# Kernel optimization log

Hardware: AMD Instinct MI355X
Metric: run time of the kernel (lower is better)

## Reference

```python
import jax, jax.numpy as jnp
import numpy as np

B, S, H, NH = 8, 2048, 128, 4
HS = H // NH
EPS = 1e-8


def setup_inputs() -> dict:
    key = jax.random.key(0)
    ks = jax.random.split(key, 20)
    sc = 1.0 / np.sqrt(H)
    d = {
        'item_embeds': jax.random.normal(ks[0], (B, S, H), jnp.float32),
        'behavior_embeds': jax.random.normal(ks[1], (B, S, H), jnp.float32),
        'attn_mask': jnp.zeros((B, 1, S, S), jnp.float32),
    }
    names = ['Wq', 'Wk', 'Wv', 'Wqb', 'Wkb', 'Wvb', 'Wf']
    for i, n in enumerate(names):
        d[n] = jax.random.normal(ks[2 + i], (H, H), jnp.float32) * sc
        d['b' + n[1:]] = jnp.zeros((H,), jnp.float32)
    d['ln_w'] = jnp.ones((H,), jnp.float32)
    d['ln_b'] = jnp.zeros((H,), jnp.float32)
    return d


def _split_heads(x):
    # [B,S,H] -> [B,NH,S,HS]
    return x.reshape(B, S, NH, HS).transpose(0, 2, 1, 3)


def _layer_norm(x, w, b):
    u = jnp.mean(x, -1, keepdims=True)
    s = jnp.mean((x - u) ** 2, -1, keepdims=True)
    return w * ((x - u) / jnp.sqrt(s + EPS)) + b


def reference(item_embeds, behavior_embeds, attn_mask,
              Wq, bq, Wk, bk, Wv, bv,
              Wqb, bqb, Wkb, bkb, Wvb, bvb,
              Wf, bf, ln_w, ln_b):
    Q = _split_heads(item_embeds @ Wq + bq)
    K = _split_heads(item_embeds @ Wk + bk)
    V = _split_heads(item_embeds @ Wv + bv)
    Qb = _split_heads(behavior_embeds @ Wqb + bqb)
    Kb = _split_heads(behavior_embeds @ Wkb + bkb)
    # V_behavior computed in the original forward but unused downstream
    _Vb = _split_heads(behavior_embeds @ Wvb + bvb)
    scores = (jnp.einsum('bhqd,bhkd->bhqk', Q, K)
              + jnp.einsum('bhqd,bhkd->bhqk', Qb, Kb)) / np.sqrt(HS)
    scores = scores + attn_mask
    probs = jax.nn.softmax(scores, axis=-1)
    attn_out = jnp.einsum('bhqk,bhkd->bhqd', probs, V)
    attn_out = attn_out.transpose(0, 2, 1, 3).reshape(B, S, H)
    out = attn_out @ Wf + bf
    return _layer_norm(out + item_embeds, ln_w, ln_b)
```

## Files before the change

kernel.cpp:

```cpp
#include <hip/hip_runtime.h>
#include <math.h>

typedef unsigned short ushort_t;
typedef __attribute__((ext_vector_type(8))) short bf16x8;
typedef __attribute__((ext_vector_type(4))) float f32x4;

namespace {
constexpr int B = 8, S = 2048, H = 128, NH = 4, HS = 32;
constexpr float EPS = 1e-8f;
constexpr float SCALE = 0.17677669529663687f;
constexpr int QT = 32, KT = 64;
constexpr int NE = B * S * H;
}

__device__ __forceinline__ ushort_t f2bf(float f) {
  unsigned u = __float_as_uint(f);
  unsigned r = (u + 0x7FFFu + ((u >> 16) & 1u)) >> 16;
  return (ushort_t)r;
}

__device__ __forceinline__ f32x4 mfma16(bf16x8 a, bf16x8 b, f32x4 c) {
  return __builtin_amdgcn_mfma_f32_16x16x32_bf16(a, b, c, 0, 0, 0);
}

__global__ __launch_bounds__(256) void wcvt_kernel(
    const float* __restrict__ Wq, const float* __restrict__ Wk, const float* __restrict__ Wv,
    const float* __restrict__ Wqb, const float* __restrict__ Wkb, const float* __restrict__ Wf,
    ushort_t* __restrict__ Wt)
{
  const float* Ws[6] = {Wq, Wk, Wv, Wqb, Wkb, Wf};
  const int m = blockIdx.y;
  const int kb = blockIdx.x;
  const float* W = Ws[m];
  __shared__ float T[32 * 132];
  const int t = threadIdx.x;
#pragma unroll
  for (int u = 0; u < 4; ++u) {
    const int idx = u * 256 + t;
    const int row = idx >> 5, c4 = idx & 31;
    const float4 v = *(const float4*)&W[(kb * 32 + row) * H + c4 * 4];
    *(float4*)&T[row * 132 + c4 * 4] = v;
  }
  __syncthreads();
#pragma unroll
  for (int u = 0; u < 16; ++u) {
    const int idx = u * 256 + t;
    const int n = idx >> 5, kk = idx & 31;
    Wt[m * (H * H) + n * H + kb * 32 + kk] = f2bf(T[kk * 132 + n]);
  }
}

__global__ __launch_bounds__(256) void proj_kernel(
    const float* __restrict__ item, const float* __restrict__ beh,
    const ushort_t* __restrict__ Wt,
    const float* __restrict__ bq, const float* __restrict__ bk, const float* __restrict__ bv,
    const float* __restrict__ bqb, const float* __restrict__ bkb,
    ushort_t* __restrict__ Qo, ushort_t* __restrict__ Ko, ushort_t* __restrict__ Qbo,
    ushort_t* __restrict__ Kbo, ushort_t* __restrict__ Vto)
{
  __shared__ ushort_t Xi[64 * 136];
  __shared__ ushort_t Xb[64 * 136];
  const int t = threadIdx.x;
  const long r0 = (long)blockIdx.x * 64;
#pragma unroll
  for (int u = 0; u < 8; ++u) {
    const int idx = u * 256 + t;
    const int row = idx >> 5, c4 = idx & 31;
    const float4 vi = *(const float4*)&item[(r0 + row) * H + c4 * 4];
    const float4 vb = *(const float4*)&beh[(r0 + row) * H + c4 * 4];
    unsigned long long pi = (unsigned long long)f2bf(vi.x) | ((unsigned long long)f2bf(vi.y) << 16)
        | ((unsigned long long)f2bf(vi.z) << 32) | ((unsigned long long)f2bf(vi.w) << 48);
    unsigned long long pb = (unsigned long long)f2bf(vb.x) | ((unsigned long long)f2bf(vb.y) << 16)
        | ((unsigned long long)f2bf(vb.z) << 32) | ((unsigned long long)f2bf(vb.w) << 48);
    *(unsigned long long*)&Xi[row * 136 + c4 * 4] = pi;
    *(unsigned long long*)&Xb[row * 136 + c4 * 4] = pb;
  }
  __syncthreads();

  const int w = t >> 6, l = t & 63, l15 = l & 15, quad = l >> 4;
  const int bb = (int)(r0 >> 11);
  const int s0 = (int)(r0 & (S - 1));
  const float* bias[5] = {bq, bk, bv, bqb, bkb};
  ushort_t* dsts[5] = {Qo, Ko, Vto, Qbo, Kbo};

  bf16x8 af[4][4];
#pragma unroll
  for (int mt = 0; mt < 4; ++mt)
#pragma unroll
    for (int ks = 0; ks < 4; ++ks)
      af[mt][ks] = *(const bf16x8*)&Xi[(mt * 16 + l15) * 136 + ks * 32 + quad * 8];

  for (int p = 0; p < 5; ++p) {
    if (p == 3) {
#pragma unroll
      for (int mt = 0; mt < 4; ++mt)
#pragma unroll
        for (int ks = 0; ks < 4; ++ks)
          af[mt][ks] = *(const bf16x8*)&Xb[(mt * 16 + l15) * 136 + ks * 32 + quad * 8];
    }
    f32x4 acc[4][2];
    float bcol[2];
#pragma unroll
    for (int nt = 0; nt < 2; ++nt) {
      bcol[nt] = bias[p][w * 32 + nt * 16 + l15];
#pragma unroll
      for (int mt = 0; mt < 4; ++mt)
        acc[mt][nt] = (f32x4){bcol[nt], bcol[nt], bcol[nt], bcol[nt]};
    }
    const ushort_t* Wp = Wt + p * (H * H);
#pragma unroll
    for (int ks = 0; ks < 4; ++ks) {
      bf16x8 bfr[2];
#pragma unroll
      for (int nt = 0; nt < 2; ++nt)
        bfr[nt] = *(const bf16x8*)&Wp[(w * 32 + nt * 16 + l15) * H + ks * 32 + quad * 8];
#pragma unroll
      for (int mt = 0; mt < 4; ++mt)
#pragma unroll
        for (int nt = 0; nt < 2; ++nt)
          acc[mt][nt] = mfma16(af[mt][ks], bfr[nt], acc[mt][nt]);
    }
    ushort_t* dst = dsts[p];
#pragma unroll
    for (int mt = 0; mt < 4; ++mt)
#pragma unroll
      for (int nt = 0; nt < 2; ++nt)
#pragma unroll
        for (int r = 0; r < 4; ++r) {
          const int s = s0 + mt * 16 + quad * 4 + r;
          const int d = nt * 16 + l15;
          long idx;
          if (p == 2)
            idx = ((long)(bb * NH + w) * HS + d) * S + s;
          else
            idx = ((long)(bb * NH + w) * S + s) * HS + d;
          dst[idx] = f2bf(acc[mt][nt][r]);
        }
  }
}

__global__ __launch_bounds__(256) void attn_kernel(
    const ushort_t* __restrict__ Q, const ushort_t* __restrict__ K,
    const ushort_t* __restrict__ Qb, const ushort_t* __restrict__ Kb,
    const ushort_t* __restrict__ Vt, const float* __restrict__ mask,
    ushort_t* __restrict__ attn_out)
{
  __shared__ ushort_t Pb[NH][32 * 72];
  const int t = threadIdx.x;
  const int w = t >> 6;
  const int l = t & 63, l15 = l & 15, quad = l >> 4;
  const int q0 = blockIdx.x * QT;
  const int b = blockIdx.y;
  const long hQ = (long)(b * NH + w) * S * HS;
  const long hV = (long)(b * NH + w) * HS * S;

  bf16x8 qf[2], qbf[2];
#pragma unroll
  for (int mt = 0; mt < 2; ++mt) {
    qf[mt]  = *(const bf16x8*)&Q[hQ + (long)(q0 + mt * 16 + l15) * HS + quad * 8];
    qbf[mt] = *(const bf16x8*)&Qb[hQ + (long)(q0 + mt * 16 + l15) * HS + quad * 8];
  }
  const float* mbase[2][4];
#pragma unroll
  for (int mt = 0; mt < 2; ++mt)
#pragma unroll
    for (int r = 0; r < 4; ++r)
      mbase[mt][r] = mask + ((long)b * S + q0 + mt * 16 + quad * 4 + r) * S + l15;

  float mold[2][4], lsum[2][4];
  f32x4 O[2][2];
#pragma unroll
  for (int mt = 0; mt < 2; ++mt) {
#pragma unroll
    for (int r = 0; r < 4; ++r) { mold[mt][r] = -1e30f; lsum[mt][r] = 0.f; }
#pragma unroll
    for (int dt = 0; dt < 2; ++dt) O[mt][dt] = (f32x4){0.f, 0.f, 0.f, 0.f};
  }
  ushort_t* Pw = Pb[w];

  for (int kt = 0; kt < S / KT; ++kt) {
    const int k0 = kt * KT;
    float mk[2][4][4];
#pragma unroll
    for (int mt = 0; mt < 2; ++mt)
#pragma unroll
      for (int r = 0; r < 4; ++r)
#pragma unroll
        for (int nt = 0; nt < 4; ++nt)
          mk[mt][nt][r] = mbase[mt][r][k0 + nt * 16];
    bf16x8 kf[4], kbf[4], vf[2][2];
#pragma unroll
    for (int nt = 0; nt < 4; ++nt) {
      kf[nt]  = *(const bf16x8*)&K[hQ + (long)(k0 + nt * 16 + l15) * HS + quad * 8];
      kbf[nt] = *(const bf16x8*)&Kb[hQ + (long)(k0 + nt * 16 + l15) * HS + quad * 8];
    }
#pragma unroll
    for (int dt = 0; dt < 2; ++dt)
#pragma unroll
      for (int ks = 0; ks < 2; ++ks)
        vf[dt][ks] = *(const bf16x8*)&Vt[hV + (long)(dt * 16 + l15) * S + k0 + ks * 32 + quad * 8];

    f32x4 sc[2][4];
#pragma unroll
    for (int mt = 0; mt < 2; ++mt)
#pragma unroll
      for (int nt = 0; nt < 4; ++nt) {
        f32x4 z = (f32x4){0.f, 0.f, 0.f, 0.f};
        z = mfma16(qf[mt], kf[nt], z);
        z = mfma16(qbf[mt], kbf[nt], z);
        sc[mt][nt] = z;
      }
#pragma unroll
    for (int mt = 0; mt < 2; ++mt)
#pragma unroll
      for (int nt = 0; nt < 4; ++nt)
#pragma unroll
        for (int r = 0; r < 4; ++r)
          sc[mt][nt][r] = sc[mt][nt][r] * SCALE + mk[mt][nt][r];
    float alpha[2][4];
#pragma unroll
    for (int mt = 0; mt < 2; ++mt)
#pragma unroll
      for (int r = 0; r < 4; ++r) {
        float rm = fmaxf(fmaxf(sc[mt][0][r], sc[mt][1][r]), fmaxf(sc[mt][2][r], sc[mt][3][r]));
        rm = fmaxf(rm, __shfl_xor(rm, 1));
        rm = fmaxf(rm, __shfl_xor(rm, 2));
        rm = fmaxf(rm, __shfl_xor(rm, 4));
        rm = fmaxf(rm, __shfl_xor(rm, 8));
        const float mnew = fmaxf(mold[mt][r], rm);
        alpha[mt][r] = __expf(mold[mt][r] - mnew);
        float rs = 0.f;
#pragma unroll
        for (int nt = 0; nt < 4; ++nt) {
          const float p = __expf(sc[mt][nt][r] - mnew);
          sc[mt][nt][r] = p;
          rs += p;
        }
        rs += __shfl_xor(rs, 1);
        rs += __shfl_xor(rs, 2);
        rs += __shfl_xor(rs, 4);
        rs += __shfl_xor(rs, 8);
        lsum[mt][r] = lsum[mt][r] * alpha[mt][r] + rs;
        mold[mt][r] = mnew;
      }
#pragma unroll
    for (int mt = 0; mt < 2; ++mt)
#pragma unroll
      for (int dt = 0; dt < 2; ++dt)
#pragma unroll
        for (int r = 0; r < 4; ++r)
          O[mt][dt][r] *= alpha[mt][r];
#pragma unroll
    for (int mt = 0; mt < 2; ++mt)
#pragma unroll
      for (int nt = 0; nt < 4; ++nt)
#pragma unroll
        for (int r = 0; r < 4; ++r)
          Pw[(mt * 16 + quad * 4 + r) * 72 + nt * 16 + l15] = f2bf(sc[mt][nt][r]);
#pragma unroll
    for (int mt = 0; mt < 2; ++mt) {
      bf16x8 pf[2];
#pragma unroll
      for (int ks = 0; ks < 2; ++ks)
        pf[ks] = *(const bf16x8*)&Pw[(mt * 16 + l15) * 72 + ks * 32 + quad * 8];
#pragma unroll
      for (int dt = 0; dt < 2; ++dt)
#pragma unroll
        for (int ks = 0; ks < 2; ++ks)
          O[mt][dt] = mfma16(pf[ks], vf[dt][ks], O[mt][dt]);
    }
  }
#pragma unroll
  for (int mt = 0; mt < 2; ++mt)
#pragma unroll
    for (int r = 0; r < 4; ++r) {
      const float inv = 1.f / lsum[mt][r];
      const long row = (long)b * S + q0 + mt * 16 + quad * 4 + r;
#pragma unroll
      for (int dt = 0; dt < 2; ++dt)
        attn_out[row * H + w * 32 + dt * 16 + l15] = f2bf(O[mt][dt][r] * inv);
    }
}

__global__ __launch_bounds__(256) void out_kernel(
    const ushort_t* __restrict__ attn, const float* __restrict__ item,
    const ushort_t* __restrict__ Wft, const float* __restrict__ bf_,
    const float* __restrict__ lnw, const float* __restrict__ lnb,
    float* __restrict__ out)
{
  __shared__ ushort_t As[64 * 136];
  __shared__ float Ys[64 * 132];
  const int t = threadIdx.x;
  const long r0 = (long)blockIdx.x * 64;
#pragma unroll
  for (int u = 0; u < 4; ++u) {
    const int idx = u * 256 + t;
    const int row = idx >> 4, c8 = idx & 15;
    *(uint4*)&As[row * 136 + c8 * 8] = *(const uint4*)&attn[(r0 + row) * H + c8 * 8];
  }
  __syncthreads();
  const int w = t >> 6, l = t & 63, l15 = l & 15, quad = l >> 4;
  f32x4 acc[4][2];
#pragma unroll
  for (int nt = 0; nt < 2; ++nt) {
    const float bcol = bf_[w * 32 + nt * 16 + l15];
#pragma unroll
    for (int mt = 0; mt < 4; ++mt)
      acc[mt][nt] = (f32x4){bcol, bcol, bcol, bcol};
  }
#pragma unroll
  for (int ks = 0; ks < 4; ++ks) {
    bf16x8 bfr[2];
#pragma unroll
    for (int nt = 0; nt < 2; ++nt)
      bfr[nt] = *(const bf16x8*)&Wft[(w * 32 + nt * 16 + l15) * H + ks * 32 + quad * 8];
#pragma unroll
    for (int mt = 0; mt < 4; ++mt) {
      const bf16x8 a = *(const bf16x8*)&As[(mt * 16 + l15) * 136 + ks * 32 + quad * 8];
      for (int nt = 0; nt < 2; ++nt)
        acc[mt][nt] = mfma16(a, bfr[nt], acc[mt][nt]);
    }
  }
#pragma unroll
  for (int mt = 0; mt < 4; ++mt)
#pragma unroll
    for (int nt = 0; nt < 2; ++nt)
#pragma unroll
      for (int r = 0; r < 4; ++r) {
        const int rl = mt * 16 + quad * 4 + r;
        const int col = w * 32 + nt * 16 + l15;
        Ys[rl * 132 + col] = acc[mt][nt][r] + item[(r0 + rl) * H + col];
      }
  __syncthreads();
  const int rl = t >> 2, ch = t & 3;
  float v[32];
#pragma unroll
  for (int g = 0; g < 8; ++g) {
    const float4 y = *(const float4*)&Ys[rl * 132 + ch * 32 + g * 4];
    v[g * 4 + 0] = y.x; v[g * 4 + 1] = y.y; v[g * 4 + 2] = y.z; v[g * 4 + 3] = y.w;
  }
  float s = 0.f;
#pragma unroll
  for (int i = 0; i < 32; ++i) s += v[i];
  s += __shfl_xor(s, 1);
  s += __shfl_xor(s, 2);
  const float u_ = s * (1.f / H);
  float s2 = 0.f;
#pragma unroll
  for (int i = 0; i < 32; ++i) { const float d = v[i] - u_; s2 += d * d; }
  s2 += __shfl_xor(s2, 1);
  s2 += __shfl_xor(s2, 2);
  const float rinv = rsqrtf(s2 * (1.f / H) + EPS);
#pragma unroll
  for (int g = 0; g < 8; ++g) {
    float4 o;
    const int col = ch * 32 + g * 4;
    o.x = lnw[col + 0] * ((v[g * 4 + 0] - u_) * rinv) + lnb[col + 0];
    o.y = lnw[col + 1] * ((v[g * 4 + 1] - u_) * rinv) + lnb[col + 1];
    o.z = lnw[col + 2] * ((v[g * 4 + 2] - u_) * rinv) + lnb[col + 2];
    o.w = lnw[col + 3] * ((v[g * 4 + 3] - u_) * rinv) + lnb[col + 3];
    *(float4*)&out[(r0 + rl) * H + col] = o;
  }
}

extern "C" void kernel_launch(void* const* d_in, const int* in_sizes, int n_in,
                              void* d_out, int out_size, void* d_ws, size_t ws_size,
                              hipStream_t stream) {
  const float* item = (const float*)d_in[0];
  const float* beh  = (const float*)d_in[1];
  const float* mask = (const float*)d_in[2];
  const float* Wq  = (const float*)d_in[3];  const float* bq  = (const float*)d_in[4];
  const float* Wk  = (const float*)d_in[5];  const float* bk  = (const float*)d_in[6];
  const float* Wv  = (const float*)d_in[7];  const float* bv  = (const float*)d_in[8];
  const float* Wqb = (const float*)d_in[9];  const float* bqb = (const float*)d_in[10];
  const float* Wkb = (const float*)d_in[11]; const float* bkb = (const float*)d_in[12];
  const float* Wf  = (const float*)d_in[15]; const float* bfv = (const float*)d_in[16];
  const float* lnw = (const float*)d_in[17]; const float* lnb = (const float*)d_in[18];
  float* out = (float*)d_out;

  ushort_t* ws = (ushort_t*)d_ws;
  ushort_t* Qw   = ws;
  ushort_t* Kw   = Qw + NE;
  ushort_t* Qbw  = Kw + NE;
  ushort_t* Kbw  = Qbw + NE;
  ushort_t* Vtw  = Kbw + NE;
  ushort_t* Attw = Vtw + NE;
  ushort_t* Wt   = Attw + NE;

  wcvt_kernel<<<dim3(4, 6), 256, 0, stream>>>(Wq, Wk, Wv, Wqb, Wkb, Wf, Wt);
  proj_kernel<<<dim3((B * S) / 64), 256, 0, stream>>>(
      item, beh, Wt, bq, bk, bv, bqb, bkb, Qw, Kw, Qbw, Kbw, Vtw);
  attn_kernel<<<dim3(S / QT, B), 256, 0, stream>>>(
      Qw, Kw, Qbw, Kbw, Vtw, mask, Attw);
  out_kernel<<<dim3((B * S) / 64), 256, 0, stream>>>(
      Attw, item, Wt + 5 * H * H, bfv, lnw, lnb, out);
}
```

Before: 380.9 us.

## Halve tile rows, fold softmax scale into weights, stage projection stores via LDS

The attention query tile drops from 32 to 16 rows, with launch bounds requesting 4 blocks per CU, so more blocks run and each uses fewer registers. The 1/sqrt(HS) scale is folded into the Wq/Wqb weights and their biases, and the mask is preloaded into the MFMA accumulator, which removes the per-score multiply-add. The projection kernel now handles 32 rows per block, keeps both input fragments resident, and stages results in LDS so global stores are 16-byte coalesced, including the transposed V. The output kernel also moves to 32-row tiles. In exchange, K/V and mask reads are repeated across twice as many query blocks, and the projection adds extra barriers.

Measured after the change: 379.4 us. Within noise of the previous version (-0.4%).

```diff
diff --git a/kernel.cpp b/kernel.cpp
--- a/kernel.cpp
+++ b/kernel.cpp
@@ -9,7 +9,7 @@
 constexpr int B = 8, S = 2048, H = 128, NH = 4, HS = 32;
 constexpr float EPS = 1e-8f;
 constexpr float SCALE = 0.17677669529663687f;
-constexpr int QT = 32, KT = 64;
+constexpr int QT = 16, KT = 64;
 constexpr int NE = B * S * H;
 }
 
@@ -29,9 +29,11 @@
     ushort_t* __restrict__ Wt)
 {
   const float* Ws[6] = {Wq, Wk, Wv, Wqb, Wkb, Wf};
+  const float scl[6] = {SCALE, 1.f, 1.f, SCALE, 1.f, 1.f};
   const int m = blockIdx.y;
   const int kb = blockIdx.x;
   const float* W = Ws[m];
+  const float sc = scl[m];
   __shared__ float T[32 * 132];
   const int t = threadIdx.x;
 #pragma unroll
@@ -46,7 +48,7 @@
   for (int u = 0; u < 16; ++u) {
     const int idx = u * 256 + t;
     const int n = idx >> 5, kk = idx & 31;
-    Wt[m * (H * H) + n * H + kb * 32 + kk] = f2bf(T[kk * 132 + n]);
+    Wt[m * (H * H) + n * H + kb * 32 + kk] = f2bf(T[kk * 132 + n] * sc);
   }
 }
 
@@ -58,12 +60,13 @@
     ushort_t* __restrict__ Qo, ushort_t* __restrict__ Ko, ushort_t* __restrict__ Qbo,
     ushort_t* __restrict__ Kbo, ushort_t* __restrict__ Vto)
 {
-  __shared__ ushort_t Xi[64 * 136];
-  __shared__ ushort_t Xb[64 * 136];
+  __shared__ ushort_t Xi[32 * 136];
+  __shared__ ushort_t Xb[32 * 136];
+  __shared__ ushort_t Yb[32 * 136];
   const int t = threadIdx.x;
-  const long r0 = (long)blockIdx.x * 64;
-#pragma unroll
-  for (int u = 0; u < 8; ++u) {
+  const long r0 = (long)blockIdx.x * 32;
+#pragma unroll
+  for (int u = 0; u < 4; ++u) {
     const int idx = u * 256 + t;
     const int row = idx >> 5, c4 = idx & 31;
     const float4 vi = *(const float4*)&item[(r0 + row) * H + c4 * 4];
@@ -81,33 +84,29 @@
   const int bb = (int)(r0 >> 11);
   const int s0 = (int)(r0 & (S - 1));
   const float* bias[5] = {bq, bk, bv, bqb, bkb};
+  const float bscale[5] = {SCALE, 1.f, 1.f, SCALE, 1.f};
   ushort_t* dsts[5] = {Qo, Ko, Vto, Qbo, Kbo};
 
-  bf16x8 af[4][4];
-#pragma unroll
-  for (int mt = 0; mt < 4; ++mt)
-#pragma unroll
-    for (int ks = 0; ks < 4; ++ks)
-      af[mt][ks] = *(const bf16x8*)&Xi[(mt * 16 + l15) * 136 + ks * 32 + quad * 8];
+  bf16x8 afi[2][4], afb[2][4];
+#pragma unroll
+  for (int mt = 0; mt < 2; ++mt)
+#pragma unroll
+    for (int ks = 0; ks < 4; ++ks) {
+      afi[mt][ks] = *(const bf16x8*)&Xi[(mt * 16 + l15) * 136 + ks * 32 + quad * 8];
+      afb[mt][ks] = *(const bf16x8*)&Xb[(mt * 16 + l15) * 136 + ks * 32 + quad * 8];
+    }
 
   for (int p = 0; p < 5; ++p) {
-    if (p == 3) {
-#pragma unroll
-      for (int mt = 0; mt < 4; ++mt)
-#pragma unroll
-        for (int ks = 0; ks < 4; ++ks)
-          af[mt][ks] = *(const bf16x8*)&Xb[(mt * 16 + l15) * 136 + ks * 32 + quad * 8];
-    }
-    f32x4 acc[4][2];
-    float bcol[2];
+    f32x4 acc[2][2];
 #pragma unroll
     for (int nt = 0; nt < 2; ++nt) {
-      bcol[nt] = bias[p][w * 32 + nt * 16 + l15];
-#pragma unroll
-      for (int mt = 0; mt < 4; ++mt)
-        acc[mt][nt] = (f32x4){bcol[nt], bcol[nt], bcol[nt], bcol[nt]};
+      const float bcol = bias[p][w * 32 + nt * 16 + l15] * bscale[p];
+#pragma unroll
+      for (int mt = 0; mt < 2; ++mt)
+        acc[mt][nt] = (f32x4){bcol, bcol, bcol, bcol};
     }
     const ushort_t* Wp = Wt + p * (H * H);
+    const bf16x8 (*af)[4] = (p < 3) ? afi : afb;
 #pragma unroll
     for (int ks = 0; ks < 4; ++ks) {
       bf16x8 bfr[2];
@@ -115,37 +114,46 @@
       for (int nt = 0; nt < 2; ++nt)
         bfr[nt] = *(const bf16x8*)&Wp[(w * 32 + nt * 16 + l15) * H + ks * 32 + quad * 8];
 #pragma unroll
-      for (int mt = 0; mt < 4; ++mt)
+      for (int mt = 0; mt < 2; ++mt)
 #pragma unroll
         for (int nt = 0; nt < 2; ++nt)
           acc[mt][nt] = mfma16(af[mt][ks], bfr[nt], acc[mt][nt]);
     }
+#pragma unroll
+    for (int mt = 0; mt < 2; ++mt)
+#pragma unroll
+      for (int nt = 0; nt < 2; ++nt)
+#pragma unroll
+        for (int r = 0; r < 4; ++r)
+          Yb[(mt * 16 + quad * 4 + r) * 136 + w * 32 + nt * 16 + l15] = f2bf(acc[mt][nt][r]);
+    __syncthreads();
     ushort_t* dst = dsts[p];
-#pragma unroll
-    for (int mt = 0; mt < 4; ++mt)
-#pragma unroll
-      for (int nt = 0; nt < 2; ++nt)
-#pragma unroll
-        for (int r = 0; r < 4; ++r) {
-          const int s = s0 + mt * 16 + quad * 4 + r;
-          const int d = nt * 16 + l15;
-          long idx;
-          if (p == 2)
-            idx = ((long)(bb * NH + w) * HS + d) * S + s;
-          else
-            idx = ((long)(bb * NH + w) * S + s) * HS + d;
-          dst[idx] = f2bf(acc[mt][nt][r]);
-        }
-  }
-}
-
-__global__ __launch_bounds__(256) void attn_kernel(
+    if (p == 2) {
+      const int d = t >> 1, sh = (t & 1) * 16;
+      ushort_t tmp[16];
+#pragma unroll
+      for (int i = 0; i < 16; ++i) tmp[i] = Yb[(sh + i) * 136 + d];
+      const long gidx = ((long)(bb * NH + (d >> 5)) * HS + (d & 31)) * S + s0 + sh;
+      *(uint4*)&dst[gidx] = *(const uint4*)&tmp[0];
+      *(uint4*)&dst[gidx + 8] = *(const uint4*)&tmp[8];
+    } else {
+      const int row = t >> 3, cb = (t & 7) * 16;
+      const int h = cb >> 5, dd = cb & 31;
+      const long gidx = ((long)(bb * NH + h) * S + s0 + row) * HS + dd;
+      *(uint4*)&dst[gidx] = *(const uint4*)&Yb[row * 136 + cb];
+      *(uint4*)&dst[gidx + 8] = *(const uint4*)&Yb[row * 136 + cb + 8];
+    }
+    __syncthreads();
+  }
+}
+
+__global__ __launch_bounds__(256, 4) void attn_kernel(
     const ushort_t* __restrict__ Q, const ushort_t* __restrict__ K,
     const ushort_t* __restrict__ Qb, const ushort_t* __restrict__ Kb,
     const ushort_t* __restrict__ Vt, const float* __restrict__ mask,
     ushort_t* __restrict__ attn_out)
 {
-  __shared__ ushort_t Pb[NH][32 * 72];
+  __shared__ ushort_t Pb[NH][16 * 72];
   const int t = threadIdx.x;
   const int w = t >> 6;
   const int l = t & 63, l15 = l & 15, quad = l >> 4;
@@ -154,40 +162,30 @@
   const long hQ = (long)(b * NH + w) * S * HS;
   const long hV = (long)(b * NH + w) * HS * S;
 
-  bf16x8 qf[2], qbf[2];
-#pragma unroll
-  for (int mt = 0; mt < 2; ++mt) {
-    qf[mt]  = *(const bf16x8*)&Q[hQ + (long)(q0 + mt * 16 + l15) * HS + quad * 8];
-    qbf[mt] = *(const bf16x8*)&Qb[hQ + (long)(q0 + mt * 16 + l15) * HS + quad * 8];
-  }
-  const float* mbase[2][4];
-#pragma unroll
-  for (int mt = 0; mt < 2; ++mt)
-#pragma unroll
-    for (int r = 0; r < 4; ++r)
-      mbase[mt][r] = mask + ((long)b * S + q0 + mt * 16 + quad * 4 + r) * S + l15;
-
-  float mold[2][4], lsum[2][4];
-  f32x4 O[2][2];
-#pragma unroll
-  for (int mt = 0; mt < 2; ++mt) {
-#pragma unroll
-    for (int r = 0; r < 4; ++r) { mold[mt][r] = -1e30f; lsum[mt][r] = 0.f; }
-#pragma unroll
-    for (int dt = 0; dt < 2; ++dt) O[mt][dt] = (f32x4){0.f, 0.f, 0.f, 0.f};
-  }
+  const bf16x8 qf  = *(const bf16x8*)&Q[hQ + (long)(q0 + l15) * HS + quad * 8];
+  const bf16x8 qbf = *(const bf16x8*)&Qb[hQ + (long)(q0 + l15) * HS + quad * 8];
+
+  const float* mrow[4];
+#pragma unroll
+  for (int r = 0; r < 4; ++r)
+    mrow[r] = mask + ((long)b * S + q0 + quad * 4 + r) * S + l15;
+
+  float mold[4], lsum[4];
+  f32x4 O[2];
+#pragma unroll
+  for (int r = 0; r < 4; ++r) { mold[r] = -1e30f; lsum[r] = 0.f; }
+#pragma unroll
+  for (int dt = 0; dt < 2; ++dt) O[dt] = (f32x4){0.f, 0.f, 0.f, 0.f};
   ushort_t* Pw = Pb[w];
 
   for (int kt = 0; kt < S / KT; ++kt) {
     const int k0 = kt * KT;
-    float mk[2][4][4];
-#pragma unroll
-    for (int mt = 0; mt < 2; ++mt)
+    f32x4 sc[4];
+#pragma unroll
+    for (int nt = 0; nt < 4; ++nt)
 #pragma unroll
       for (int r = 0; r < 4; ++r)
-#pragma unroll
-        for (int nt = 0; nt < 4; ++nt)
-          mk[mt][nt][r] = mbase[mt][r][k0 + nt * 16];
+        sc[nt][r] = mrow[r][k0 + nt * 16];
     bf16x8 kf[4], kbf[4], vf[2][2];
 #pragma unroll
     for (int nt = 0; nt < 4; ++nt) {
@@ -199,87 +197,63 @@
 #pragma unroll
       for (int ks = 0; ks < 2; ++ks)
         vf[dt][ks] = *(const bf16x8*)&Vt[hV + (long)(dt * 16 + l15) * S + k0 + ks * 32 + quad * 8];
-
-    f32x4 sc[2][4];
-#pragma unroll
-    for (int mt = 0; mt < 2; ++mt)
+#pragma unroll
+    for (int nt = 0; nt < 4; ++nt) {
+      sc[nt] = mfma16(qbf, kbf[nt], sc[nt]);
+      sc[nt] = mfma16(qf, kf[nt], sc[nt]);
+    }
+    float alpha[4];
+#pragma unroll
+    for (int r = 0; r < 4; ++r) {
+      float rm = fmaxf(fmaxf(sc[0][r], sc[1][r]), fmaxf(sc[2][r], sc[3][r]));
+      rm = fmaxf(rm, __shfl_xor(rm, 1));
+      rm = fmaxf(rm, __shfl_xor(rm, 2));
+      rm = fmaxf(rm, __shfl_xor(rm, 4));
+      rm = fmaxf(rm, __shfl_xor(rm, 8));
+      const float mnew = fmaxf(mold[r], rm);
+      alpha[r] = __expf(mold[r] - mnew);
+      float rs = 0.f;
 #pragma unroll
       for (int nt = 0; nt < 4; ++nt) {
-        f32x4 z = (f32x4){0.f, 0.f, 0.f, 0.f};
-        z = mfma16(qf[mt], kf[nt], z);
-        z = mfma16(qbf[mt], kbf[nt], z);
-        sc[mt][nt] = z;
+        const float p = __expf(sc[nt][r] - mnew);
+        sc[nt][r] = p;
+        rs += p;
       }
-#pragma unroll
-    for (int mt = 0; mt < 2; ++mt)
-#pragma unroll
-      for (int nt = 0; nt < 4; ++nt)
-#pragma unroll
-        for (int r = 0; r < 4; ++r)
-          sc[mt][nt][r] = sc[mt][nt][r] * SCALE + mk[mt][nt][r];
-    float alpha[2][4];
-#pragma unroll
-    for (int mt = 0; mt < 2; ++mt)
-#pragma unroll
-      for (int r = 0; r < 4; ++r) {
-        float rm = fmaxf(fmaxf(sc[mt][0][r], sc[mt][1][r]), fmaxf(sc[mt][2][r], sc[mt][3][r]));
-        rm = fmaxf(rm, __shfl_xor(rm, 1));
-        rm = fmaxf(rm, __shfl_xor(rm, 2));
-        rm = fmaxf(rm, __shfl_xor(rm, 4));
-        rm = fmaxf(rm, __shfl_xor(rm, 8));
-        const float mnew = fmaxf(mold[mt][r], rm);
-        alpha[mt][r] = __expf(mold[mt][r] - mnew);
-        float rs = 0.f;
-#pragma unroll
-        for (int nt = 0; nt < 4; ++nt) {
-          const float p = __expf(sc[mt][nt][r] - mnew);
-          sc[mt][nt][r] = p;
-          rs += p;
-        }
-        rs += __shfl_xor(rs, 1);
-        rs += __shfl_xor(rs, 2);
-        rs += __shfl_xor(rs, 4);
-        rs += __shfl_xor(rs, 8);
-        lsum[mt][r] = lsum[mt][r] * alpha[mt][r] + rs;
-        mold[mt][r] = mnew;
-      }
-#pragma unroll
-    for (int mt = 0; mt < 2; ++mt)
-#pragma unroll
-      for (int dt = 0; dt < 2; ++dt)
-#pragma unroll
-        for (int r = 0; r < 4; ++r)
-          O[mt][dt][r] *= alpha[mt][r];
-#pragma unroll
-    for (int mt = 0; mt < 2; ++mt)
-#pragma unroll
-      for (int nt = 0; nt < 4; ++nt)
-#pragma unroll
-        for (int r = 0; r < 4; ++r)
-          Pw[(mt * 16 + quad * 4 + r) * 72 + nt * 16 + l15] = f2bf(sc[mt][nt][r]);
-#pragma unroll
-    for (int mt = 0; mt < 2; ++mt) {
-      bf16x8 pf[2];
+      rs += __shfl_xor(rs, 1);
+      rs += __shfl_xor(rs, 2);
+      rs += __shfl_xor(rs, 4);
+      rs += __shfl_xor(rs, 8);
+      lsum[r] = lsum[r] * alpha[r] + rs;
+      mold[r] = mnew;
+    }
+#pragma unroll
+    for (int dt = 0; dt < 2; ++dt)
+#pragma unroll
+      for (int r = 0; r < 4; ++r)
+        O[dt][r] *= alpha[r];
+#pragma unroll
+    for (int nt = 0; nt < 4; ++nt)
+#pragma unroll
+      for (int r = 0; r < 4; ++r)
+        Pw[(quad * 4 + r) * 72 + nt * 16 + l15] = f2bf(sc[nt][r]);
+    bf16x8 pf[2];
+#pragma unroll
+    for (int ks = 0; ks < 2; ++ks)
+      pf[ks] = *(const bf16x8*)&Pw[l15 * 72 + ks * 32 + quad * 8];
+#pragma unroll
+    for (int dt = 0; dt < 2; ++dt)
 #pragma unroll
       for (int ks = 0; ks < 2; ++ks)
-        pf[ks] = *(const bf16x8*)&Pw[(mt * 16 + l15) * 72 + ks * 32 + quad * 8];
-#pragma unroll
-      for (int dt = 0; dt < 2; ++dt)
-#pragma unroll
-        for (int ks = 0; ks < 2; ++ks)
-          O[mt][dt] = mfma16(pf[ks], vf[dt][ks], O[mt][dt]);
-    }
-  }
-#pragma unroll
-  for (int mt = 0; mt < 2; ++mt)
-#pragma unroll
-    for (int r = 0; r < 4; ++r) {
-      const float inv = 1.f / lsum[mt][r];
-      const long row = (long)b * S + q0 + mt * 16 + quad * 4 + r;
-#pragma unroll
-      for (int dt = 0; dt < 2; ++dt)
-        attn_out[row * H + w * 32 + dt * 16 + l15] = f2bf(O[mt][dt][r] * inv);
-    }
+        O[dt] = mfma16(pf[ks], vf[dt][ks], O[dt]);
+  }
+#pragma unroll
+  for (int r = 0; r < 4; ++r) {
+    const float inv = 1.f / lsum[r];
+    const long row = (long)b * S + q0 + quad * 4 + r;
+#pragma unroll
+    for (int dt = 0; dt < 2; ++dt)
+      attn_out[row * H + w * 32 + dt * 16 + l15] = f2bf(O[dt][r] * inv);
+  }
 }
 
 __global__ __launch_bounds__(256) void out_kernel(
@@ -288,24 +262,24 @@
     const float* __restrict__ lnw, const float* __restrict__ lnb,
     float* __restrict__ out)
 {
-  __shared__ ushort_t As[64 * 136];
-  __shared__ float Ys[64 * 132];
+  __shared__ ushort_t As[32 * 136];
+  __shared__ float Ys[32 * 132];
   const int t = threadIdx.x;
-  const long r0 = (long)blockIdx.x * 64;
-#pragma unroll
-  for (int u = 0; u < 4; ++u) {
+  const long r0 = (long)blockIdx.x * 32;
+#pragma unroll
+  for (int u = 0; u < 2; ++u) {
     const int idx = u * 256 + t;
     const int row = idx >> 4, c8 = idx & 15;
     *(uint4*)&As[row * 136 + c8 * 8] = *(const uint4*)&attn[(r0 + row) * H + c8 * 8];
   }
   __syncthreads();
   const int w = t >> 6, l = t & 63, l15 = l & 15, quad = l >> 4;
-  f32x4 acc[4][2];
+  f32x4 acc[2][2];
 #pragma unroll
   for (int nt = 0; nt < 2; ++nt) {
     const float bcol = bf_[w * 32 + nt * 16 + l15];
 #pragma unroll
-    for (int mt = 0; mt < 4; ++mt)
+    for (int mt = 0; mt < 2; ++mt)
       acc[mt][nt] = (f32x4){bcol, bcol, bcol, bcol};
   }
 #pragma unroll
@@ -315,14 +289,15 @@
     for (int nt = 0; nt < 2; ++nt)
       bfr[nt] = *(const bf16x8*)&Wft[(w * 32 + nt * 16 + l15) * H + ks * 32 + quad * 8];
 #pragma unroll
-    for (int mt = 0; mt < 4; ++mt) {
+    for (int mt = 0; mt < 2; ++mt) {
       const bf16x8 a = *(const bf16x8*)&As[(mt * 16 + l15) * 136 + ks * 32 + quad * 8];
+#pragma unroll
       for (int nt = 0; nt < 2; ++nt)
         acc[mt][nt] = mfma16(a, bfr[nt], acc[mt][nt]);
     }
   }
 #pragma unroll
-  for (int mt = 0; mt < 4; ++mt)
+  for (int mt = 0; mt < 2; ++mt)
 #pragma unroll
     for (int nt = 0; nt < 2; ++nt)
 #pragma unroll
@@ -332,29 +307,31 @@
         Ys[rl * 132 + col] = acc[mt][nt][r] + item[(r0 + rl) * H + col];
       }
   __syncthreads();
-  const int rl = t >> 2, ch = t & 3;
-  float v[32];
-#pragma unroll
-  for (int g = 0; g < 8; ++g) {
-    const float4 y = *(const float4*)&Ys[rl * 132 + ch * 32 + g * 4];
+  const int rl = t >> 3, ch = t & 7;
+  float v[16];
+#pragma unroll
+  for (int g = 0; g < 4; ++g) {
+    const float4 y = *(const float4*)&Ys[rl * 132 + ch * 16 + g * 4];
     v[g * 4 + 0] = y.x; v[g * 4 + 1] = y.y; v[g * 4 + 2] = y.z; v[g * 4 + 3] = y.w;
   }
   float s = 0.f;
 #pragma unroll
-  for (int i = 0; i < 32; ++i) s += v[i];
+  for (int i = 0; i < 16; ++i) s += v[i];
   s += __shfl_xor(s, 1);
   s += __shfl_xor(s, 2);
+  s += __shfl_xor(s, 4);
   const float u_ = s * (1.f / H);
   float s2 = 0.f;
 #pragma unroll
-  for (int i = 0; i < 32; ++i) { const float d = v[i] - u_; s2 += d * d; }
+  for (int i = 0; i < 16; ++i) { const float d = v[i] - u_; s2 += d * d; }
   s2 += __shfl_xor(s2, 1);
   s2 += __shfl_xor(s2, 2);
+  s2 += __shfl_xor(s2, 4);
   const float rinv = rsqrtf(s2 * (1.f / H) + EPS);
 #pragma unroll
-  for (int g = 0; g < 8; ++g) {
+  for (int g = 0; g < 4; ++g) {
     float4 o;
-    const int col = ch * 32 + g * 4;
+    const int col = ch * 16 + g * 4;
     o.x = lnw[col + 0] * ((v[g * 4 + 0] - u_) * rinv) + lnb[col + 0];
     o.y = lnw[col + 1] * ((v[g * 4 + 1] - u_) * rinv) + lnb[col + 1];
     o.z = lnw[col + 2] * ((v[g * 4 + 2] - u_) * rinv) + lnb[col + 2];
@@ -388,10 +365,10 @@
   ushort_t* Wt   = Attw + NE;
 
   wcvt_kernel<<<dim3(4, 6), 256, 0, stream>>>(Wq, Wk, Wv, Wqb, Wkb, Wf, Wt);
-  proj_kernel<<<dim3((B * S) / 64), 256, 0, stream>>>(
+  proj_kernel<<<dim3((B * S) / 32), 256, 0, stream>>>(
       item, beh, Wt, bq, bk, bv, bqb, bkb, Qw, Kw, Qbw, Kbw, Vtw);
   attn_kernel<<<dim3(S / QT, B), 256, 0, stream>>>(
       Qw, Kw, Qbw, Kbw, Vtw, mask, Attw);
-  out_kernel<<<dim3((B * S) / 64), 256, 0, stream>>>(
+  out_kernel<<<dim3((B * S) / 32), 256, 0, stream>>>(
       Attw, item, Wt + 5 * H * H, bfv, lnw, lnb, out);
 }
```
